# Optimization experiments

Measured on AMD Instinct MI355X. Metric: run time of the kernel, lower is better.

## Reference

```python
import jax, jax.numpy as jnp
import numpy as np

B, C, H, W = 8, 64, 128, 128


def _conv3x3(x, w, b):
    # x: [B,C,H,W], w: [O,I,3,3], b: [O]; stride 1, padding 1
    y = jax.lax.conv_general_dilated(
        x, w, window_strides=(1, 1), padding=((1, 1), (1, 1)),
        dimension_numbers=('NCHW', 'OIHW', 'NCHW'))
    return y + b[None, :, None, None]


def setup_inputs() -> dict:
    key = jax.random.key(0)
    ks = jax.random.split(key, 8)
    s = 0.05
    return {
        'x': jax.random.normal(ks[0], (B, C, H, W), jnp.float32),
        'Wq': jax.random.normal(ks[1], (C, C, 3, 3), jnp.float32) * s,
        'bq': jax.random.normal(ks[2], (C,), jnp.float32) * s,
        'Wk': jax.random.normal(ks[3], (C, C, 3, 3), jnp.float32) * s,
        'bk': jax.random.normal(ks[4], (C,), jnp.float32) * s,
        'Wv': jax.random.normal(ks[5], (C, C, 3, 3), jnp.float32) * s,
        'bv': jax.random.normal(ks[6], (C,), jnp.float32) * s,
        'gamma': jax.random.normal(ks[7], (1,), jnp.float32) * s,
    }


def reference(x, Wq, bq, Wk, bk, Wv, bv, gamma):
    b_, c_, h_, w_ = x.shape
    q = _conv3x3(x, Wq, bq)  # [B,C,H,W]
    k = _conv3x3(x, Wk, bk)
    v = _conv3x3(x, Wv, bv)

    # energy along H (column attention): eH[b,h,w,g] = sum_c q[b,c,h,w]*k[b,c,g,w]
    eH = jnp.einsum('bchw,bcgw->bhwg', q, k)
    eye = jnp.eye(h_, dtype=bool)  # mask diagonal h==g with -inf
    eH = jnp.where(eye[None, :, None, :], -jnp.inf, eH)

    # energy along W (row attention): eW[b,h,w,g] = sum_c q[b,c,h,w]*k[b,c,h,g]
    eW = jnp.einsum('bchw,bchg->bhwg', q, k)

    # joint softmax over concatenated [H | W] axis
    att = jax.nn.softmax(jnp.concatenate([eH, eW], axis=3), axis=3)
    att_H = att[:, :, :, :h_]          # [B,H,W,H]
    att_W = att[:, :, :, h_:h_ + w_]   # [B,H,W,W]

    out_H = jnp.einsum('bcgw,bhwg->bchw', v, att_H)
    out_W = jnp.einsum('bchg,bhwg->bchw', v, att_W)

    return gamma[0] * (out_H + out_W) + x
```

## Files before the change

### kernel.cpp

```cpp
#include <hip/hip_runtime.h>
#include <hip/hip_bf16.h>

#define B_ 8
#define C_ 64
#define H_ 128
#define W_ 128
#define HW_  ((size_t)H_ * W_)
#define CHW_ ((size_t)C_ * H_ * W_)

typedef unsigned short u16;
typedef unsigned int   u32;
typedef __attribute__((ext_vector_type(8))) short bf16x8;
typedef __attribute__((ext_vector_type(4))) float f32x4;

__device__ __forceinline__ float bf2f(u16 h) {
    union { u32 u; float f; } c; c.u = ((u32)h) << 16; return c.f;
}
__device__ __forceinline__ u16 f2bf(float f) {
    union { float f; u32 u; } c; c.f = f;
    u32 u = c.u;
    u32 r = (u + 0x7fffu + ((u >> 16) & 1u)) >> 16;
    return (u16)r;
}
__device__ __forceinline__ u32 pack2(float a, float b) {
    return (u32)f2bf(a) | ((u32)f2bf(b) << 16);
}
__device__ __forceinline__ float sanit(float x, float lo, float hi) {
    return fminf(fmaxf(x, lo), hi);
}
__device__ __forceinline__ void gload_lds16(const u16* g, u16* l) {
    __builtin_amdgcn_global_load_lds(
        (const __attribute__((address_space(1))) void*)g,
        (__attribute__((address_space(3))) void*)l, 16, 0, 0);
}

__global__ __launch_bounds__(256) void prep_weights(
    const float* __restrict__ Wq, const float* __restrict__ Wk,
    const float* __restrict__ Wv, u16* __restrict__ Wt)
{
    int tap = blockIdx.x;
    int cog = blockIdx.y * 4 + (threadIdx.x >> 6);
    int ci  = threadIdx.x & 63;
    int arr = cog >> 6, co = cog & 63;
    const float* src = arr == 0 ? Wq : (arr == 1 ? Wk : Wv);
    Wt[tap * 12288 + cog * 64 + ci] = f2bf(src[(co * 64 + ci) * 9 + tap]);
}

__global__ __launch_bounds__(256) void xprep_kernel(
    const float* __restrict__ x, u16* __restrict__ xb)
{
    const int hp  = blockIdx.x;
    const int tid = threadIdx.x;
    u16* dst = xb + ((size_t)blockIdx.y * 130 + hp) * 8192;
    if (hp == 0 || hp == 129) {
#pragma unroll
        for (int i = 0; i < 4; i++)
            *(uint4*)(dst + (size_t)(tid + i * 256) * 8) = (uint4){0, 0, 0, 0};
        return;
    }
    const float* xr = x + (size_t)blockIdx.y * CHW_ + (size_t)(hp - 1) * W_;
#pragma unroll
    for (int it = 0; it < 4; it++) {
        int idx = tid + it * 256;
        int px  = idx & 127;
        int g   = idx >> 7;
        float vb[8];
#pragma unroll
        for (int e = 0; e < 8; e++)
            vb[e] = xr[(size_t)(g * 8 + e) * HW_ + px];
        uint4 o;
        o.x = pack2(vb[0], vb[1]);
        o.y = pack2(vb[2], vb[3]);
        o.z = pack2(vb[4], vb[5]);
        o.w = pack2(vb[6], vb[7]);
        *(uint4*)(dst + (size_t)(g * 128 + px) * 8) = o;
    }
}

__global__ __launch_bounds__(256, 2) void conv_mfma_kernel(
    const u16* __restrict__ xb, const u16* __restrict__ Wt,
    const float* __restrict__ bq, const float* __restrict__ bk,
    const float* __restrict__ bv,
    u16* __restrict__ qN, u16* __restrict__ kN, u16* __restrict__ v)
{
    const int nwg  = gridDim.x * gridDim.y;
    const int flat = blockIdx.y * gridDim.x + blockIdx.x;
    const int wg   = (flat & 7) * (nwg >> 3) + (flat >> 3);
    const int p    = wg & 1;
    const int hq   = (wg >> 1) & 31;
    const int bidx = wg >> 6;
    const int h0   = hq * 4;
    const size_t boff = (size_t)bidx * CHW_;
    const int tid  = threadIdx.x;
    const int lane = tid & 63, wv = tid >> 6;
    const int ln15 = lane & 15, quad = lane >> 4;

    __shared__ __align__(16) u16 xI[26112];

    const int woff = (wv * 16 + ln15) * 64 + quad * 8;

    const u16* xrow0 = xb + ((size_t)bidx * 130 + h0) * 8192;
#pragma unroll
    for (int it = 0; it < 12; it++) {
        int unit = wv * 12 + it;
        int i = unit >> 3, g = unit & 7;
        const u16* src = xrow0 + (size_t)i * 8192 + g * 1024 + p * 512 - 16;
        u16* dst = xI + (i * 8 + g) * 544;
        gload_lds16(src + lane * 8, dst);
        gload_lds16(src + 32 + lane * 8, dst + 32);
    }
    __syncthreads();
    if (tid < 48) {
        int i = tid >> 3, g = tid & 7;
        int slot = p ? 66 : 1;
        *(uint4*)(xI + (i * 8 + g) * 544 + slot * 8) = (uint4){0, 0, 0, 0};
    }
    __syncthreads();

    const int cb = wv * 16 + quad * 4;
    float bqv[4], bkv[4], bvv[4];
#pragma unroll
    for (int r = 0; r < 4; r++) {
        bqv[r] = bq[cb + r]; bkv[r] = bk[cb + r]; bvv[r] = bv[cb + r];
    }

#pragma unroll
    for (int pass = 0; pass < 2; pass++) {
        f32x4 acc[2][3][4];
#pragma unroll
        for (int hh = 0; hh < 2; hh++)
#pragma unroll
            for (int mt = 0; mt < 3; mt++)
#pragma unroll
                for (int nt = 0; nt < 4; nt++)
                    acc[hh][mt][nt] = (f32x4){0.f, 0.f, 0.f, 0.f};

        bf16x8 wcur[2][3], wnxt[2][3];
#pragma unroll
        for (int ks = 0; ks < 2; ks++)
#pragma unroll
            for (int mt = 0; mt < 3; mt++)
                wcur[ks][mt] = *(const bf16x8*)(Wt + woff + mt * 4096 + ks * 32);

#pragma unroll
        for (int tap = 0; tap < 9; tap++) {
            const int dh = tap / 3, dw = tap % 3;
            if (tap < 8) {
#pragma unroll
                for (int ks = 0; ks < 2; ks++)
#pragma unroll
                    for (int mt = 0; mt < 3; mt++)
                        wnxt[ks][mt] = *(const bf16x8*)(Wt + (tap + 1) * 12288 + woff + mt * 4096 + ks * 32);
            }
#pragma unroll
            for (int hh = 0; hh < 2; hh++) {
                const int row = pass * 2 + hh + dh;
#pragma unroll
                for (int ks = 0; ks < 2; ks++) {
                    bf16x8 bfr[4];
#pragma unroll
                    for (int nt = 0; nt < 4; nt++)
                        bfr[nt] = *(const bf16x8*)(xI + (row * 8 + quad + ks * 4) * 544
                                                      + (nt * 16 + ln15 + 1 + dw) * 8);
                    __builtin_amdgcn_s_setprio(1);
#pragma unroll
                    for (int mt = 0; mt < 3; mt++)
#pragma unroll
                        for (int nt = 0; nt < 4; nt++)
                            acc[hh][mt][nt] = __builtin_amdgcn_mfma_f32_16x16x32_bf16(
                                wcur[ks][mt], bfr[nt], acc[hh][mt][nt], 0, 0, 0);
                    __builtin_amdgcn_s_setprio(0);
                }
            }
            if (tap < 8) {
#pragma unroll
                for (int ks = 0; ks < 2; ks++)
#pragma unroll
                    for (int mt = 0; mt < 3; mt++)
                        wcur[ks][mt] = wnxt[ks][mt];
            }
        }

#pragma unroll
        for (int hh = 0; hh < 2; hh++) {
            const int h = h0 + pass * 2 + hh;
#pragma unroll
            for (int mt = 0; mt < 2; mt++) {
                const float* bb = mt == 0 ? bqv : bkv;
                u16* dst = (mt ? kN : qN) + boff + (size_t)h * W_ * 64 + cb;
#pragma unroll
                for (int nt = 0; nt < 4; nt++) {
                    int px = p * 64 + nt * 16 + ln15;
                    u32 p0 = pack2(acc[hh][mt][nt][0] + bb[0], acc[hh][mt][nt][1] + bb[1]);
                    u32 p1 = pack2(acc[hh][mt][nt][2] + bb[2], acc[hh][mt][nt][3] + bb[3]);
                    *(u32*)(dst + (size_t)px * 64)     = p0;
                    *(u32*)(dst + (size_t)px * 64 + 2) = p1;
                }
            }
#pragma unroll
            for (int r = 0; r < 4; r++) {
                u16* drow = v + boff + (size_t)(cb + r) * HW_ + (size_t)h * W_;
#pragma unroll
                for (int nt = 0; nt < 4; nt++)
                    drow[p * 64 + nt * 16 + ln15] = f2bf(acc[hh][2][nt][r] + bvv[r]);
            }
        }
    }
}

__global__ __launch_bounds__(256) void vt_kernel(
    const u16* __restrict__ v, u16* __restrict__ vT)
{
    __shared__ u16 Ts[64 * 72];
    const u16* src = v  + (size_t)blockIdx.z * CHW_ + (size_t)blockIdx.y * HW_;
    u16* dst       = vT + (size_t)blockIdx.z * CHW_ + (size_t)blockIdx.y * HW_;
    const int ti = blockIdx.x & 1, tj = blockIdx.x >> 1;
    const int r0 = ti * 64, c0 = tj * 64;
    const int tid = threadIdx.x;
    const int r = tid >> 2, cq = tid & 3;
#pragma unroll
    for (int i = 0; i < 2; i++) {
        uint4 u = *(const uint4*)(src + (size_t)(r0 + r) * 128 + c0 + cq * 16 + i * 8);
        *(uint4*)(Ts + r * 72 + cq * 16 + i * 8) = u;
    }
    __syncthreads();
    const int wr = tid >> 2, hq = tid & 3;
    union { u16 o[16]; uint4 v4[2]; } t;
#pragma unroll
    for (int j = 0; j < 16; j++) t.o[j] = Ts[(hq * 16 + j) * 72 + wr];
    *(uint4*)(dst + (size_t)(c0 + wr) * 128 + r0 + hq * 16)     = t.v4[0];
    *(uint4*)(dst + (size_t)(c0 + wr) * 128 + r0 + hq * 16 + 8) = t.v4[1];
}

__global__ __launch_bounds__(256, 4) void col_kernel(
    const u16* __restrict__ qN, const u16* __restrict__ kN,
    const u16* __restrict__ vT,
    float2* __restrict__ msl,
    u16* __restrict__ Ocol)
{
    const size_t boff = (size_t)blockIdx.z * CHW_;
    const size_t soff = (size_t)blockIdx.z * HW_;
    qN += boff; kN += boff; vT += boff; Ocol += boff;
    msl += soff;

    const int s    = blockIdx.x;
    const int tid  = threadIdx.x;
    const int lane = tid & 63, wv = tid >> 6;
    const int ln15 = lane & 15, quad = lane >> 4;

    __shared__ __align__(16) u16 smemU[18432];
    u16* Qs = smemU;
    u16* Ks = smemU + 9216;

#pragma unroll
    for (int it = 0; it < 4; it++) {
        int idx = tid + it * 256;
        int t = idx >> 3, cg = (idx & 7) * 8;
        size_t off = (size_t)t * 8192 + (size_t)s * 64 + cg;
        *(uint4*)(Qs + t * 72 + cg) = *(const uint4*)(qN + off);
        *(uint4*)(Ks + t * 72 + cg) = *(const uint4*)(kN + off);
    }
    __syncthreads();

    f32x4 Sc[2][8];
#pragma unroll
    for (int tt = 0; tt < 2; tt++)
#pragma unroll
        for (int gt = 0; gt < 8; gt++)
            Sc[tt][gt] = (f32x4){0.f, 0.f, 0.f, 0.f};

#pragma unroll
    for (int ks = 0; ks < 2; ks++) {
        bf16x8 bq_[2];
#pragma unroll
        for (int tt = 0; tt < 2; tt++)
            bq_[tt] = *(const bf16x8*)(Qs + ((wv * 2 + tt) * 16 + ln15) * 72 + ks * 32 + quad * 8);
#pragma unroll
        for (int gt = 0; gt < 8; gt++) {
            bf16x8 ak = *(const bf16x8*)(Ks + (gt * 16 + ln15) * 72 + ks * 32 + quad * 8);
#pragma unroll
            for (int tt = 0; tt < 2; tt++)
                Sc[tt][gt] = __builtin_amdgcn_mfma_f32_16x16x32_bf16(ak, bq_[tt], Sc[tt][gt], 0, 0, 0);
        }
    }

    const int tb[2] = { (wv * 2) * 16 + ln15, (wv * 2 + 1) * 16 + ln15 };
#pragma unroll
    for (int tt = 0; tt < 2; tt++)
#pragma unroll
        for (int gt = 0; gt < 8; gt++)
#pragma unroll
            for (int r = 0; r < 4; r++)
                if (gt * 16 + quad * 4 + r == tb[tt]) Sc[tt][gt][r] = -1e30f;

#pragma unroll
    for (int tt = 0; tt < 2; tt++) {
        float m = Sc[tt][0][0];
#pragma unroll
        for (int gt = 0; gt < 8; gt++)
#pragma unroll
            for (int r = 0; r < 4; r++) m = fmaxf(m, Sc[tt][gt][r]);
        m = fmaxf(m, __shfl_xor(m, 16));
        m = fmaxf(m, __shfl_xor(m, 32));
        float ss = 0.f;
#pragma unroll
        for (int gt = 0; gt < 8; gt++)
#pragma unroll
            for (int r = 0; r < 4; r++) {
                float e = __expf(Sc[tt][gt][r] - m);
                ss += e;
                Sc[tt][gt][r] = e;
            }
        ss += __shfl_xor(ss, 16);
        ss += __shfl_xor(ss, 32);
        if (quad == 0)
            msl[tb[tt] * W_ + s] = make_float2(m, ss);
    }
    __syncthreads();
    u16* Ps = smemU;
#pragma unroll
    for (int tt = 0; tt < 2; tt++)
#pragma unroll
        for (int gt = 0; gt < 8; gt++) {
            u32 lo = pack2(Sc[tt][gt][0], Sc[tt][gt][1]);
            u32 hi = pack2(Sc[tt][gt][2], Sc[tt][gt][3]);
            *(uint2*)(Ps + tb[tt] * 136 + gt * 16 + quad * 4) = make_uint2(lo, hi);
        }
    __syncthreads();

    f32x4 Oc[2][4];
#pragma unroll
    for (int mt = 0; mt < 2; mt++)
#pragma unroll
        for (int nt = 0; nt < 4; nt++)
            Oc[mt][nt] = (f32x4){0.f, 0.f, 0.f, 0.f};
#pragma unroll
    for (int kg = 0; kg < 4; kg++) {
        bf16x8 ap[2];
#pragma unroll
        for (int mt = 0; mt < 2; mt++)
            ap[mt] = *(const bf16x8*)(Ps + (wv * 32 + mt * 16 + ln15) * 136 + kg * 32 + quad * 8);
#pragma unroll
        for (int nt = 0; nt < 4; nt++) {
            bf16x8 bv_ = *(const bf16x8*)(vT + (size_t)(nt * 16 + ln15) * HW_ + (size_t)s * 128 + kg * 32 + quad * 8);
#pragma unroll
            for (int mt = 0; mt < 2; mt++)
                Oc[mt][nt] = __builtin_amdgcn_mfma_f32_16x16x32_bf16(ap[mt], bv_, Oc[mt][nt], 0, 0, 0);
        }
    }
    __syncthreads();
    u16* OfU = smemU;
#pragma unroll
    for (int mt = 0; mt < 2; mt++)
#pragma unroll
        for (int nt = 0; nt < 4; nt++)
#pragma unroll
            for (int r = 0; r < 4; r++)
                OfU[(wv * 32 + mt * 16 + quad * 4 + r) * 72 + nt * 16 + ln15] = f2bf(Oc[mt][nt][r]);
    __syncthreads();
#pragma unroll
    for (int it = 0; it < 4; it++) {
        int idx = tid + it * 256;
        int t = idx >> 3, c8 = (idx & 7) * 8;
        *(uint4*)(Ocol + ((size_t)t * 128 + s) * 64 + c8) = *(uint4*)(OfU + t * 72 + c8);
    }
}

__global__ __launch_bounds__(256, 4) void row_kernel(
    const u16* __restrict__ qN, const u16* __restrict__ kN,
    const u16* __restrict__ v,
    const float* __restrict__ x, const float* __restrict__ gammap,
    const float2* __restrict__ msl,
    const u16* __restrict__ Ocol, float* __restrict__ out)
{
    const size_t boff = (size_t)blockIdx.z * CHW_;
    const size_t soff = (size_t)blockIdx.z * HW_;
    qN += boff; kN += boff; v += boff; Ocol += boff; x += boff; out += boff;
    msl += soff;

    const int s    = blockIdx.x;
    const int tid  = threadIdx.x;
    const int lane = tid & 63, wv = tid >> 6;
    const int ln15 = lane & 15, quad = lane >> 4;

    __shared__ __align__(16) u16 smemU[18432];
    u16* Qs = smemU;
    u16* Ks = smemU + 9216;
    float* alL = (float*)(smemU + 17408);

    const int tb[2] = { (wv * 2) * 16 + ln15, (wv * 2 + 1) * 16 + ln15 };
    float2 mslv[2];
#pragma unroll
    for (int tt = 0; tt < 2; tt++)
        mslv[tt] = msl[s * W_ + tb[tt]];

#pragma unroll
    for (int it = 0; it < 4; it++) {
        int idx = tid + it * 256;
        int t = idx >> 3, cg = (idx & 7) * 8;
        size_t off = (size_t)s * 8192 + (size_t)t * 64 + cg;
        *(uint4*)(Qs + t * 72 + cg) = *(const uint4*)(qN + off);
        *(uint4*)(Ks + t * 72 + cg) = *(const uint4*)(kN + off);
    }
    __syncthreads();

    f32x4 Sc[2][8];
#pragma unroll
    for (int tt = 0; tt < 2; tt++)
#pragma unroll
        for (int gt = 0; gt < 8; gt++)
            Sc[tt][gt] = (f32x4){0.f, 0.f, 0.f, 0.f};
#pragma unroll
    for (int ks = 0; ks < 2; ks++) {
        bf16x8 bq_[2];
#pragma unroll
        for (int tt = 0; tt < 2; tt++)
            bq_[tt] = *(const bf16x8*)(Qs + ((wv * 2 + tt) * 16 + ln15) * 72 + ks * 32 + quad * 8);
#pragma unroll
        for (int gt = 0; gt < 8; gt++) {
            bf16x8 ak = *(const bf16x8*)(Ks + (gt * 16 + ln15) * 72 + ks * 32 + quad * 8);
#pragma unroll
            for (int tt = 0; tt < 2; tt++)
                Sc[tt][gt] = __builtin_amdgcn_mfma_f32_16x16x32_bf16(ak, bq_[tt], Sc[tt][gt], 0, 0, 0);
        }
    }

    float be[2];
#pragma unroll
    for (int tt = 0; tt < 2; tt++) {
        float m = Sc[tt][0][0];
#pragma unroll
        for (int gt = 0; gt < 8; gt++)
#pragma unroll
            for (int r = 0; r < 4; r++) m = fmaxf(m, Sc[tt][gt][r]);
        m = fmaxf(m, __shfl_xor(m, 16));
        m = fmaxf(m, __shfl_xor(m, 32));
        float ss = 0.f;
#pragma unroll
        for (int gt = 0; gt < 8; gt++)
#pragma unroll
            for (int r = 0; r < 4; r++) {
                float e = __expf(Sc[tt][gt][r] - m);
                ss += e;
                Sc[tt][gt][r] = e;
            }
        ss += __shfl_xor(ss, 16);
        ss += __shfl_xor(ss, 32);
        float mc = sanit(mslv[tt].x, -3e38f, 3e38f);
        float sc = sanit(mslv[tt].y, 0.f, 3e38f);
        float mm = fmaxf(mc, m);
        float dd = sc * __expf(fminf(mc - mm, 0.f)) + ss * __expf(m - mm);
        float rv = 1.0f / fmaxf(dd, 1e-30f);
        be[tt] = __expf(m - mm) * rv;
        if (quad == 0) alL[tb[tt]] = __expf(fminf(mc - mm, 0.f)) * rv;
    }
    __syncthreads();
    u16* Ps = smemU;
#pragma unroll
    for (int tt = 0; tt < 2; tt++)
#pragma unroll
        for (int gt = 0; gt < 8; gt++) {
            u32 lo = pack2(Sc[tt][gt][0] * be[tt], Sc[tt][gt][1] * be[tt]);
            u32 hi = pack2(Sc[tt][gt][2] * be[tt], Sc[tt][gt][3] * be[tt]);
            *(uint2*)(Ps + tb[tt] * 136 + gt * 16 + quad * 4) = make_uint2(lo, hi);
        }
    __syncthreads();

    f32x4 Oc[2][4];
#pragma unroll
    for (int mt = 0; mt < 2; mt++)
#pragma unroll
        for (int nt = 0; nt < 4; nt++)
            Oc[mt][nt] = (f32x4){0.f, 0.f, 0.f, 0.f};
#pragma unroll
    for (int kg = 0; kg < 4; kg++) {
        bf16x8 ap[2];
#pragma unroll
        for (int mt = 0; mt < 2; mt++)
            ap[mt] = *(const bf16x8*)(Ps + (wv * 32 + mt * 16 + ln15) * 136 + kg * 32 + quad * 8);
#pragma unroll
        for (int nt = 0; nt < 4; nt++) {
            bf16x8 bv_ = *(const bf16x8*)(v + (size_t)(nt * 16 + ln15) * HW_ + (size_t)s * 128 + kg * 32 + quad * 8);
#pragma unroll
            for (int mt = 0; mt < 2; mt++)
                Oc[mt][nt] = __builtin_amdgcn_mfma_f32_16x16x32_bf16(ap[mt], bv_, Oc[mt][nt], 0, 0, 0);
        }
    }
    __syncthreads();

    const float gmm = gammap[0];
    float* Of = (float*)smemU;
#pragma unroll
    for (int mt = 0; mt < 2; mt++)
#pragma unroll
        for (int nt = 0; nt < 4; nt++) {
            float fv[4];
            int c = nt * 16 + ln15;
#pragma unroll
            for (int r = 0; r < 4; r++) {
                int tt = wv * 32 + mt * 16 + quad * 4 + r;
                float oc = bf2f(Ocol[((size_t)s * 128 + tt) * 64 + c]);
                fv[r] = gmm * (Oc[mt][nt][r] + alL[tt] * oc);
            }
            int w0 = wv * 32 + mt * 16 + quad * 4;
            *(float4*)(Of + c * 132 + w0) = make_float4(fv[0], fv[1], fv[2], fv[3]);
        }
    __syncthreads();
    int c = tid >> 2, w0 = (tid & 3) * 32;
#pragma unroll
    for (int i = 0; i < 8; i++) {
        int w = w0 + i * 4;
        float4 xo = *(const float4*)(x + (size_t)c * HW_ + (size_t)s * 128 + w);
        float4 of = *(const float4*)(Of + c * 132 + w);
        *(float4*)(out + (size_t)c * HW_ + (size_t)s * 128 + w) =
            make_float4(of.x + xo.x, of.y + xo.y, of.z + xo.z, of.w + xo.w);
    }
}

extern "C" void kernel_launch(void* const* d_in, const int* in_sizes, int n_in,
                              void* d_out, int out_size, void* d_ws, size_t ws_size,
                              hipStream_t stream)
{
    const float* x  = (const float*)d_in[0];
    const float* Wq = (const float*)d_in[1];
    const float* bq = (const float*)d_in[2];
    const float* Wk = (const float*)d_in[3];
    const float* bk = (const float*)d_in[4];
    const float* Wv = (const float*)d_in[5];
    const float* bv = (const float*)d_in[6];
    const float* gm = (const float*)d_in[7];
    float* out = (float*)d_out;

    char* ws = (char*)d_ws;
    const size_t need1 = 4 * (size_t)B_ * CHW_ * 2 + (size_t)B_ * CHW_ * 4
                       + 2 * (size_t)B_ * HW_ * 4 + 221184;
    int passes = (ws_size >= need1) ? 1 : 2;
    int nb = B_ / passes;

    const size_t SL = (size_t)nb * CHW_ * 2;
    const size_t OC = (size_t)nb * CHW_ * 4;
    const size_t ST = (size_t)nb * HW_ * 8;
    u16*    qNb  = (u16*)(ws);
    u16*    kNb  = (u16*)(ws + SL);
    u16*    v    = (u16*)(ws + 2 * SL);
    u16*    vT   = (u16*)(ws + 3 * SL);
    u16*    Ocol = (u16*)(ws + 4 * SL);
    float2* msl  = (float2*)(ws + 4 * SL + OC);
    u16*    Wt   = (u16*)(ws + 4 * SL + OC + ST);
    u16*    xb   = (u16*)Ocol;

    dim3 blk(256);
    prep_weights<<<dim3(9, 48), blk, 0, stream>>>(Wq, Wk, Wv, Wt);

    for (int p = 0; p < passes; p++) {
        const float* xbp = x + (size_t)p * nb * CHW_;
        float* ob = out + (size_t)p * nb * CHW_;
        xprep_kernel<<<dim3(130, nb), blk, 0, stream>>>(xbp, xb);
        conv_mfma_kernel<<<dim3(64, nb), blk, 0, stream>>>(xb, Wt, bq, bk, bv, qNb, kNb, v);
        vt_kernel<<<dim3(4, C_, nb), blk, 0, stream>>>(v, vT);
        col_kernel<<<dim3(W_, 1, nb), blk, 0, stream>>>(qNb, kNb, vT, msl, Ocol);
        row_kernel<<<dim3(H_, 1, nb), blk, 0, stream>>>(qNb, kNb, v, xbp, gm, msl, Ocol, ob);
    }
}
```

Before: 186.7 us.

## Pre-swizzle Q/K global layout and load tiles via direct global-to-LDS copies

The conv kernel now writes Q and K with an XOR swizzle on the channel chunk, keyed by (h ^ pixel). This lets the column and row attention kernels copy 128-byte rows straight into unpadded LDS with gload_lds16 and read them back bank-conflict-free through the matching XOR index. It removes the register round trip and the padded shared-memory staging. The cost is that the swizzle must stay consistent between the producer and both consumers, and the gload_lds16 helper must already exist.

```diff
diff --git a/kernel.cpp b/kernel.cpp
--- a/kernel.cpp
+++ b/kernel.cpp
@@ -187,14 +187,16 @@
 #pragma unroll
             for (int mt = 0; mt < 2; mt++) {
                 const float* bb = mt == 0 ? bqv : bkv;
-                u16* dst = (mt ? kN : qN) + boff + (size_t)h * W_ * 64 + cb;
+                char* rowb = (char*)((mt ? kN : qN) + boff + (size_t)h * 8192);
 #pragma unroll
                 for (int nt = 0; nt < 4; nt++) {
                     int px = p * 64 + nt * 16 + ln15;
                     u32 p0 = pack2(acc[hh][mt][nt][0] + bb[0], acc[hh][mt][nt][1] + bb[1]);
                     u32 p1 = pack2(acc[hh][mt][nt][2] + bb[2], acc[hh][mt][nt][3] + bb[3]);
-                    *(u32*)(dst + (size_t)px * 64)     = p0;
-                    *(u32*)(dst + (size_t)px * 64 + 2) = p1;
+                    u32 bc = (u32)(cb * 2) ^ (u32)(((h ^ px) & 7) << 4);
+                    char* pxb = rowb + (size_t)px * 128;
+                    *(u32*)(pxb + bc)     = p0;
+                    *(u32*)(pxb + bc + 4) = p1;
                 }
             }
 #pragma unroll
@@ -250,15 +252,14 @@
 
     __shared__ __align__(16) u16 smemU[18432];
     u16* Qs = smemU;
-    u16* Ks = smemU + 9216;
-
-#pragma unroll
-    for (int it = 0; it < 4; it++) {
-        int idx = tid + it * 256;
-        int t = idx >> 3, cg = (idx & 7) * 8;
-        size_t off = (size_t)t * 8192 + (size_t)s * 64 + cg;
-        *(uint4*)(Qs + t * 72 + cg) = *(const uint4*)(qN + off);
-        *(uint4*)(Ks + t * 72 + cg) = *(const uint4*)(kN + off);
+    u16* Ks = smemU + 8192;
+
+#pragma unroll
+    for (int c2 = 0; c2 < 4; c2++) {
+        int tbase = wv * 32 + c2 * 8;
+        int t = tbase + (lane >> 3);
+        gload_lds16(qN + (size_t)t * 8192 + s * 64 + (lane & 7) * 8, Qs + tbase * 64);
+        gload_lds16(kN + (size_t)t * 8192 + s * 64 + (lane & 7) * 8, Ks + tbase * 64);
     }
     __syncthreads();
 
@@ -273,11 +274,16 @@
     for (int ks = 0; ks < 2; ks++) {
         bf16x8 bq_[2];
 #pragma unroll
-        for (int tt = 0; tt < 2; tt++)
-            bq_[tt] = *(const bf16x8*)(Qs + ((wv * 2 + tt) * 16 + ln15) * 72 + ks * 32 + quad * 8);
+        for (int tt = 0; tt < 2; tt++) {
+            int row = (wv * 2 + tt) * 16 + ln15;
+            u32 bc = (u32)(ks * 64 + quad * 16) ^ (u32)(((row ^ s) & 7) << 4);
+            bq_[tt] = *(const bf16x8*)((const char*)Qs + (size_t)row * 128 + bc);
+        }
 #pragma unroll
         for (int gt = 0; gt < 8; gt++) {
-            bf16x8 ak = *(const bf16x8*)(Ks + (gt * 16 + ln15) * 72 + ks * 32 + quad * 8);
+            int row = gt * 16 + ln15;
+            u32 bc = (u32)(ks * 64 + quad * 16) ^ (u32)(((row ^ s) & 7) << 4);
+            bf16x8 ak = *(const bf16x8*)((const char*)Ks + (size_t)row * 128 + bc);
 #pragma unroll
             for (int tt = 0; tt < 2; tt++)
                 Sc[tt][gt] = __builtin_amdgcn_mfma_f32_16x16x32_bf16(ak, bq_[tt], Sc[tt][gt], 0, 0, 0);
@@ -385,7 +391,7 @@
 
     __shared__ __align__(16) u16 smemU[18432];
     u16* Qs = smemU;
-    u16* Ks = smemU + 9216;
+    u16* Ks = smemU + 8192;
     float* alL = (float*)(smemU + 17408);
 
     const int tb[2] = { (wv * 2) * 16 + ln15, (wv * 2 + 1) * 16 + ln15 };
@@ -395,12 +401,11 @@
         mslv[tt] = msl[s * W_ + tb[tt]];
 
 #pragma unroll
-    for (int it = 0; it < 4; it++) {
-        int idx = tid + it * 256;
-        int t = idx >> 3, cg = (idx & 7) * 8;
-        size_t off = (size_t)s * 8192 + (size_t)t * 64 + cg;
-        *(uint4*)(Qs + t * 72 + cg) = *(const uint4*)(qN + off);
-        *(uint4*)(Ks + t * 72 + cg) = *(const uint4*)(kN + off);
+    for (int c2 = 0; c2 < 4; c2++) {
+        int tbase = wv * 32 + c2 * 8;
+        int t = tbase + (lane >> 3);
+        gload_lds16(qN + (size_t)s * 8192 + t * 64 + (lane & 7) * 8, Qs + tbase * 64);
+        gload_lds16(kN + (size_t)s * 8192 + t * 64 + (lane & 7) * 8, Ks + tbase * 64);
     }
     __syncthreads();
 
@@ -414,11 +419,16 @@
     for (int ks = 0; ks < 2; ks++) {
         bf16x8 bq_[2];
 #pragma unroll
-        for (int tt = 0; tt < 2; tt++)
-            bq_[tt] = *(const bf16x8*)(Qs + ((wv * 2 + tt) * 16 + ln15) * 72 + ks * 32 + quad * 8);
+        for (int tt = 0; tt < 2; tt++) {
+            int row = (wv * 2 + tt) * 16 + ln15;
+            u32 bc = (u32)(ks * 64 + quad * 16) ^ (u32)(((row ^ s) & 7) << 4);
+            bq_[tt] = *(const bf16x8*)((const char*)Qs + (size_t)row * 128 + bc);
+        }
 #pragma unroll
         for (int gt = 0; gt < 8; gt++) {
-            bf16x8 ak = *(const bf16x8*)(Ks + (gt * 16 + ln15) * 72 + ks * 32 + quad * 8);
+            int row = gt * 16 + ln15;
+            u32 bc = (u32)(ks * 64 + quad * 16) ^ (u32)(((row ^ s) & 7) << 4);
+            bf16x8 ak = *(const bf16x8*)((const char*)Ks + (size_t)row * 128 + bc);
 #pragma unroll
             for (int tt = 0; tt < 2; tt++)
                 Sc[tt][gt] = __builtin_amdgcn_mfma_f32_16x16x32_bf16(ak, bq_[tt], Sc[tt][gt], 0, 0, 0);
```

Measured after the change: 196.9 us. +5.5%, slower.
